# Kernel optimization log

Hardware: AMD Instinct MI355X
Metric: run time of the kernel (lower is better)

Reference implementation:

```python
import jax, jax.numpy as jnp
import numpy as np
from jax import lax

N_OBJ = 21   # 20 VOC classes + background
N_ACT = 27   # HICO actions
HUMAN = 14   # index of 'human' in VOC_BBOX_LABEL_NAMES
ROI_SZ = 7
SCALE = 1.0 / 16.0
STD = (0.1, 0.1, 0.2, 0.2)
MEAN = (0.0, 0.0, 0.0, 0.0)
SIGMA = 0.3
NMS_T = 0.0  # thresh passed to non_maximum_suppression in source
EPS = 1e-3
NEG = -1e30


def setup_inputs():
    key = jax.random.key(0)
    ks = jax.random.split(key, 9)
    R = 2000
    C, Hf, Wf = 512, 38, 50
    Himg, Wimg = 608, 800
    x = jax.random.normal(ks[0], (1, C, Hf, Wf), dtype=jnp.float32)
    pred_scores = jax.random.normal(ks[1], (R, N_OBJ), dtype=jnp.float32)
    pred_off = 0.5 * jax.random.normal(ks[2], (R, N_OBJ * 4), dtype=jnp.float32)
    ys = jnp.sort(jax.random.uniform(ks[3], (R, 2), minval=0.0, maxval=Himg - 1.0), axis=1)
    xs = jnp.sort(jax.random.uniform(ks[4], (R, 2), minval=0.0, maxval=Wimg - 1.0), axis=1)
    rois = jnp.stack([ys[:, 0], xs[:, 0], ys[:, 1] + 1.0, xs[:, 1] + 1.0], axis=1)  # [R,4] yxyx, image coords
    D = C * ROI_SZ * ROI_SZ  # 25088
    W1 = jax.random.normal(ks[5], (D, 4096), dtype=jnp.float32) / np.float32(np.sqrt(D))
    b1 = jnp.zeros((4096,), jnp.float32)
    W2 = jax.random.normal(ks[6], (4096, 4096), dtype=jnp.float32) / 64.0
    b2 = jnp.zeros((4096,), jnp.float32)
    W_loc = jax.random.normal(ks[7], (4096, 4), dtype=jnp.float32) / 64.0
    b_loc = jnp.zeros((4,), jnp.float32)
    W_act = jax.random.normal(ks[8], (4096, N_ACT), dtype=jnp.float32) / 64.0
    b_act = jnp.zeros((N_ACT,), jnp.float32)
    imgshape = jnp.array([Himg, Wimg], dtype=jnp.int32)
    return {"x": x, "pred_scores": pred_scores, "pred_off": pred_off, "rois": rois,
            "imgshape": imgshape, "W1": W1, "b1": b1, "W2": W2, "b2": b2,
            "W_loc": W_loc, "b_loc": b_loc, "W_act": W_act, "b_act": b_act}


def loc2bbox(src, loc):
    # src, loc: [...,4] (y1,x1,y2,x2) / (dy,dx,dh,dw)
    h = src[..., 2] - src[..., 0]
    w = src[..., 3] - src[..., 1]
    cy = src[..., 0] + 0.5 * h
    cx = src[..., 1] + 0.5 * w
    cy2 = loc[..., 0] * h + cy
    cx2 = loc[..., 1] * w + cx
    h2 = jnp.exp(loc[..., 2]) * h
    w2 = jnp.exp(loc[..., 3]) * w
    return jnp.stack([cy2 - 0.5 * h2, cx2 - 0.5 * w2, cy2 + 0.5 * h2, cx2 + 0.5 * w2], axis=-1)


def nms_keep(boxes, scores):
    # chainercv-style greedy NMS: suppress if IoU with an already-kept box >= NMS_T
    R = boxes.shape[0]
    order = jnp.argsort(-scores)
    b = boxes[order]
    tl = jnp.maximum(b[:, None, :2], b[None, :, :2])
    br = jnp.minimum(b[:, None, 2:], b[None, :, 2:])
    inter = jnp.prod(jnp.maximum(br - tl, 0.0), axis=-1)
    area = jnp.prod(jnp.maximum(b[:, 2:] - b[:, :2], 0.0), axis=-1)
    iou = inter / (area[:, None] + area[None, :] - inter + 1e-12)
    idx = jnp.arange(R)
    def body(i, keep):
        sup = jnp.any((iou[i] >= NMS_T) & keep & (idx < i))
        return keep.at[i].set(~sup)
    keep_sorted = lax.fori_loop(0, R, body, jnp.ones((R,), bool))
    return jnp.zeros((R,), bool).at[order].set(keep_sorted)


def roi_pool(feat, box_yxyx):
    # chainer RoIPooling2D on one roi; roi fed as [x1,y1,x2,y2] then scaled by SCALE
    C, Hf, Wf = feat.shape
    y1, x1, y2, x2 = box_yxyx[0], box_yxyx[1], box_yxyx[2], box_yxyx[3]
    xmin = jnp.round(x1 * SCALE).astype(jnp.int32)
    ymin = jnp.round(y1 * SCALE).astype(jnp.int32)
    xmax = jnp.round(x2 * SCALE).astype(jnp.int32)
    ymax = jnp.round(y2 * SCALE).astype(jnp.int32)
    rw = jnp.maximum(xmax - xmin + 1, 1).astype(jnp.float32)
    rh = jnp.maximum(ymax - ymin + 1, 1).astype(jnp.float32)
    p = jnp.arange(ROI_SZ, dtype=jnp.float32)
    hstart = jnp.clip(ymin + jnp.floor(p * rh / ROI_SZ).astype(jnp.int32), 0, Hf)
    hend = jnp.clip(ymin + jnp.ceil((p + 1.0) * rh / ROI_SZ).astype(jnp.int32), 0, Hf)
    wstart = jnp.clip(xmin + jnp.floor(p * rw / ROI_SZ).astype(jnp.int32), 0, Wf)
    wend = jnp.clip(xmin + jnp.ceil((p + 1.0) * rw / ROI_SZ).astype(jnp.int32), 0, Wf)
    r = jnp.arange(Hf)
    c = jnp.arange(Wf)
    rowm = (r[None, :] >= hstart[:, None]) & (r[None, :] < hend[:, None])  # [7,Hf]
    colm = (c[None, :] >= wstart[:, None]) & (c[None, :] < wend[:, None])  # [7,Wf]
    t = jnp.where(colm[None, None, :, :], feat[:, :, None, :], NEG).max(axis=-1)  # [C,Hf,7]
    out = jnp.where(rowm[None, :, :, None], t[:, None, :, :], NEG).max(axis=2)    # [C,7,7]
    return jnp.where(out <= NEG * 0.5, 0.0, out)


def xywh(b):
    # quirky encoding used in forward: x=(b3-b1)/2, y=(b2-b0)/2, w=b3-b1, h=b2-b0
    w = b[..., 3] - b[..., 1]
    h = b[..., 2] - b[..., 0]
    return jnp.stack([0.5 * w, 0.5 * h, w, h], axis=-1)


def reference(x, pred_scores, pred_off, rois, imgshape, W1, b1, W2, b2, W_loc, b_loc, W_act, b_act):
    Hf, Wf = x.shape[2], x.shape[3]
    R = rois.shape[0]
    img = imgshape.astype(jnp.float32)
    my_scale = Hf / img[0]
    sy = Hf / img[0]
    sx = Wf / img[1]
    roi = rois * jnp.stack([sy, sx, sy, sx])  # resize_bbox(image -> feature)
    std = jnp.tile(jnp.asarray(STD, jnp.float32), (N_OBJ,))
    mean = jnp.tile(jnp.asarray(MEAN, jnp.float32), (N_OBJ,))
    loc = (pred_off * std + mean).reshape(R, N_OBJ, 4)
    src = jnp.broadcast_to(roi[:, None, :], loc.shape)
    cb = loc2bbox(src, loc)  # [R,21,4]
    yc = jnp.clip(cb[..., 0::2], 0.0, float(Hf))
    xc = jnp.clip(cb[..., 1::2], 0.0, float(Wf))
    cls_bbox = jnp.stack([yc[..., 0], xc[..., 0], yc[..., 1], xc[..., 1]], axis=-1)
    prob = jax.nn.softmax(pred_scores, axis=1)  # strictly > 0, so prob>0 mask keeps all
    boxes_c = jnp.swapaxes(cls_bbox[:, 1:, :], 0, 1)  # [20,R,4]
    scores_c = prob[:, 1:].T                          # [20,R]
    keep = jax.vmap(nms_keep)(boxes_c, scores_c)      # [20,R] bool
    bbox_all = boxes_c.reshape(-1, 4)
    score_all = scores_c.reshape(-1)
    label_all = jnp.repeat(jnp.arange(N_OBJ - 1), R)
    kept = keep.reshape(-1)
    # get_pred_human_box: best-scoring kept box with label 'human'
    hmask = kept & (label_all == HUMAN)
    hi = jnp.argmax(jnp.where(hmask, score_all, -1.0))
    human_box = bbox_all[hi]  # feature coords, yxyx
    # RoI pool + classifier heads
    pool = roi_pool(x[0], human_box)
    feat = pool.reshape(1, -1)  # [1, 25088]
    fc7 = jax.nn.relu(jax.nn.relu(feat @ W1 + b1) @ W2 + b2)
    pred_object_loc = fc7 @ W_loc + b_loc   # [1,4]
    action_scores = fc7 @ W_act + b_act     # [1,27]
    # test-mode: gaussian over relative box encodings to pick object
    h4 = xywh(human_box)
    mu = xywh(pred_object_loc[0])
    cand = xywh(bbox_all)  # [20R,4]
    hw = jnp.maximum(h4[2], EPS)
    hh = jnp.maximum(h4[3], EPS)
    cw = jnp.maximum(cand[:, 2], EPS)
    ch = jnp.maximum(cand[:, 3], EPS)
    boh = jnp.stack([(cand[:, 0] - h4[0]) / hw, (cand[:, 1] - h4[1]) / hh,
                     jnp.log(cw / hw), jnp.log(ch / hh)], axis=-1)
    gau = jnp.exp(-jnp.sum((boh - mu) ** 2, axis=-1) / (2.0 * SIGMA * SIGMA))
    vmask = kept & (label_all != HUMAN)
    bi = jnp.argmax(jnp.where(vmask, gau, -1.0))
    obj_box = bbox_all[bi]
    # resize back to image coords (flip_bbox treated as identity)
    inv = jnp.stack([img[0] / Hf, img[1] / Wf, img[0] / Hf, img[1] / Wf])
    pred_human_box = (human_box * inv)[None, :]
    pred_obj_box = (obj_box * inv)[None, :]
    return pred_human_box, pred_obj_box, action_scores, my_scale
```

## Files before the change

kernel.cpp:

```cpp
#include <hip/hip_runtime.h>
#include <math.h>

#define R_ROIS 2000
#define NOBJ   21
#define NACT   27
#define HUMAN  14
#define CFEAT  512
#define HF     38
#define WF     50
#define DFEAT  (CFEAT*7*7)
#define H1DIM  4096

typedef float floatx4 __attribute__((ext_vector_type(4)));

#define WS_KEPT   0
#define WS_FEAT   80
#define WS_H1     (WS_FEAT + DFEAT)
#define WS_FC7    (WS_H1 + H1DIM)
#define WS_LOC    (WS_FC7 + H1DIM)
#define WS_ACT    (WS_LOC + 4)

__global__ __launch_bounds__(256)
void k_top(const float* __restrict__ scores, const float* __restrict__ off,
           const float* __restrict__ rois, const int* __restrict__ imgshape,
           float* __restrict__ kept_box, float* __restrict__ h1,
           float* __restrict__ fc7) {
    int g = blockIdx.x * 256 + threadIdx.x;
    for (int j = g; j < 2 * H1DIM; j += 20 * 256) {
        if (j < H1DIM) h1[j] = 0.f; else fc7[j - H1DIM] = 0.f;
    }

    int cls = blockIdx.x + 1;
    __shared__ float sval[256];
    __shared__ int   sidx[256];
    float best = -1e30f; int bidx = 0x7fffffff;
    for (int r = threadIdx.x; r < R_ROIS; r += 256) {
        const float* s = scores + r * NOBJ;
        float m = s[0];
        #pragma unroll
        for (int c = 1; c < NOBJ; ++c) m = fmaxf(m, s[c]);
        float sum = 0.f;
        #pragma unroll
        for (int c = 0; c < NOBJ; ++c) sum += expf(s[c] - m);
        float v = s[cls] - (m + logf(sum));
        if (v > best) { best = v; bidx = r; }
    }
    sval[threadIdx.x] = best; sidx[threadIdx.x] = bidx;
    __syncthreads();
    for (int s = 128; s > 0; s >>= 1) {
        if (threadIdx.x < s) {
            float ov = sval[threadIdx.x + s]; int oi = sidx[threadIdx.x + s];
            if (ov > sval[threadIdx.x] ||
                (ov == sval[threadIdx.x] && oi < sidx[threadIdx.x])) {
                sval[threadIdx.x] = ov; sidx[threadIdx.x] = oi;
            }
        }
        __syncthreads();
    }
    if (threadIdx.x == 0) {
        int r = sidx[0];
        float Himg = (float)imgshape[0], Wimg = (float)imgshape[1];
        float sy = (float)HF / Himg, sx = (float)WF / Wimg;
        float y1 = rois[r*4+0]*sy, x1 = rois[r*4+1]*sx;
        float y2 = rois[r*4+2]*sy, x2 = rois[r*4+3]*sx;
        float dy = off[r*(NOBJ*4) + cls*4+0] * 0.1f;
        float dx = off[r*(NOBJ*4) + cls*4+1] * 0.1f;
        float dh = off[r*(NOBJ*4) + cls*4+2] * 0.2f;
        float dw = off[r*(NOBJ*4) + cls*4+3] * 0.2f;
        float h = y2 - y1, w = x2 - x1;
        float cy = y1 + 0.5f*h, cx = x1 + 0.5f*w;
        float cy2 = dy*h + cy, cx2 = dx*w + cx;
        float h2 = expf(dh)*h, w2 = expf(dw)*w;
        float by1 = fminf(fmaxf(cy2 - 0.5f*h2, 0.f), (float)HF);
        float bx1 = fminf(fmaxf(cx2 - 0.5f*w2, 0.f), (float)WF);
        float by2 = fminf(fmaxf(cy2 + 0.5f*h2, 0.f), (float)HF);
        float bx2 = fminf(fmaxf(cx2 + 0.5f*w2, 0.f), (float)WF);
        int l = cls - 1;
        kept_box[l*4+0] = by1; kept_box[l*4+1] = bx1;
        kept_box[l*4+2] = by2; kept_box[l*4+3] = bx2;
    }
}

__global__ void k_roipool(const float* __restrict__ x, const float* __restrict__ kept_box,
                          float* __restrict__ feat) {
    int idx = blockIdx.x * blockDim.x + threadIdx.x;
    if (idx >= DFEAT) return;
    float y1 = kept_box[HUMAN*4+0], x1 = kept_box[HUMAN*4+1];
    float y2 = kept_box[HUMAN*4+2], x2 = kept_box[HUMAN*4+3];
    int xmin = (int)rintf(x1 * 0.0625f);
    int ymin = (int)rintf(y1 * 0.0625f);
    int xmax = (int)rintf(x2 * 0.0625f);
    int ymax = (int)rintf(y2 * 0.0625f);
    float rw = (float)max(xmax - xmin + 1, 1);
    float rh = (float)max(ymax - ymin + 1, 1);
    int c = idx / 49, rem = idx % 49, pi = rem / 7, pj = rem % 7;
    int hs  = min(max(ymin + (int)floorf((float)pi * rh / 7.f), 0), HF);
    int he  = min(max(ymin + (int)ceilf((float)(pi+1) * rh / 7.f), 0), HF);
    int wss = min(max(xmin + (int)floorf((float)pj * rw / 7.f), 0), WF);
    int we  = min(max(xmin + (int)ceilf((float)(pj+1) * rw / 7.f), 0), WF);
    float m = -1e30f;
    for (int rr = hs; rr < he; ++rr)
        for (int cc = wss; cc < we; ++cc)
            m = fmaxf(m, x[c*(HF*WF) + rr*WF + cc]);
    feat[idx] = (m <= -5e29f) ? 0.f : m;
}

template<int ROWS, bool RELU>
__global__ __launch_bounds__(256)
void k_matvec(const float* __restrict__ W, const float* __restrict__ vin,
              const float* __restrict__ bias, float* __restrict__ vout, int ncols) {
    __shared__ float sv[ROWS];
    int row0 = blockIdx.x * ROWS;
    int col0 = blockIdx.y * 1024 + threadIdx.x * 4;
    for (int i = threadIdx.x; i < ROWS; i += 256) {
        float v = vin[row0 + i];
        if (RELU) v = fmaxf(v + bias[row0 + i], 0.f);
        sv[i] = v;
    }
    __syncthreads();
    float a0 = 0.f, a1 = 0.f, a2 = 0.f, a3 = 0.f;
    const floatx4* Wv = (const floatx4*)W;
    long base = ((long)row0 * ncols + col0) >> 2;
    int stride = ncols >> 2;
    #pragma unroll 8
    for (int i = 0; i < ROWS; ++i) {
        float f = sv[i];
        floatx4 w = __builtin_nontemporal_load(&Wv[base + (long)i * stride]);
        a0 += f * w.x; a1 += f * w.y; a2 += f * w.z; a3 += f * w.w;
    }
    atomicAdd(&vout[col0+0], a0);
    atomicAdd(&vout[col0+1], a1);
    atomicAdd(&vout[col0+2], a2);
    atomicAdd(&vout[col0+3], a3);
}

__global__ void k_heads(const float* __restrict__ fc7, const float* __restrict__ b2,
                        const float* __restrict__ W_loc, const float* __restrict__ b_loc,
                        const float* __restrict__ W_act, const float* __restrict__ b_act,
                        float* __restrict__ loc_out, float* __restrict__ act_out) {
    int k = blockIdx.x;
    __shared__ float red[256];
    float sum = 0.f;
    if (k < 4) {
        for (int i = threadIdx.x; i < H1DIM; i += 256) {
            float f = fmaxf(fc7[i] + b2[i], 0.f);
            sum += f * W_loc[i*4 + k];
        }
    } else {
        int j = k - 4;
        for (int i = threadIdx.x; i < H1DIM; i += 256) {
            float f = fmaxf(fc7[i] + b2[i], 0.f);
            sum += f * W_act[i*NACT + j];
        }
    }
    red[threadIdx.x] = sum; __syncthreads();
    for (int s = 128; s > 0; s >>= 1) {
        if (threadIdx.x < s) red[threadIdx.x] += red[threadIdx.x + s];
        __syncthreads();
    }
    if (threadIdx.x == 0) {
        if (k < 4) loc_out[k] = red[0] + b_loc[k];
        else       act_out[k-4] = red[0] + b_act[k-4];
    }
}

__global__ void k_final(const float* __restrict__ kept_box, const float* __restrict__ loc_out,
                        const float* __restrict__ act_out, const int* __restrict__ imgshape,
                        float* __restrict__ out) {
    if (threadIdx.x != 0 || blockIdx.x != 0) return;
    float hb0 = kept_box[HUMAN*4+0], hb1 = kept_box[HUMAN*4+1];
    float hb2 = kept_box[HUMAN*4+2], hb3 = kept_box[HUMAN*4+3];
    float h4w = hb3 - hb1, h4h = hb2 - hb0;
    float h4x = 0.5f * h4w, h4y = 0.5f * h4h;
    float hw = fmaxf(h4w, 1e-3f), hh = fmaxf(h4h, 1e-3f);
    float l0 = loc_out[0], l1 = loc_out[1], l2 = loc_out[2], l3 = loc_out[3];
    float muw = l3 - l1, muh = l2 - l0;
    float mux = 0.5f * muw, muy = 0.5f * muh;
    float bestg = -2.f; int bl = 0;
    for (int l = 0; l < 20; ++l) {
        if (l == HUMAN) continue;
        float b0 = kept_box[l*4+0], b1 = kept_box[l*4+1];
        float b2 = kept_box[l*4+2], b3 = kept_box[l*4+3];
        float cw = fmaxf(b3 - b1, 1e-3f), ch = fmaxf(b2 - b0, 1e-3f);
        float c0 = 0.5f * (b3 - b1), c1 = 0.5f * (b2 - b0);
        float d0 = (c0 - h4x) / hw - mux;
        float d1 = (c1 - h4y) / hh - muy;
        float d2 = logf(cw / hw) - muw;
        float d3 = logf(ch / hh) - muh;
        float g = expf(-(d0*d0 + d1*d1 + d2*d2 + d3*d3) / (2.f * 0.3f * 0.3f));
        if (g > bestg) { bestg = g; bl = l; }
    }
    float Himg = (float)imgshape[0], Wimg = (float)imgshape[1];
    float iy = Himg / (float)HF, ix = Wimg / (float)WF;
    out[0] = hb0 * iy; out[1] = hb1 * ix; out[2] = hb2 * iy; out[3] = hb3 * ix;
    out[4] = kept_box[bl*4+0] * iy; out[5] = kept_box[bl*4+1] * ix;
    out[6] = kept_box[bl*4+2] * iy; out[7] = kept_box[bl*4+3] * ix;
    for (int j = 0; j < NACT; ++j) out[8+j] = act_out[j];
    out[35] = (float)HF / Himg;
}

extern "C" void kernel_launch(void* const* d_in, const int* in_sizes, int n_in,
                              void* d_out, int out_size, void* d_ws, size_t ws_size,
                              hipStream_t stream) {
    const float* x           = (const float*)d_in[0];
    const float* pred_scores = (const float*)d_in[1];
    const float* pred_off    = (const float*)d_in[2];
    const float* rois        = (const float*)d_in[3];
    const int*   imgshape    = (const int*)d_in[4];
    const float* W1          = (const float*)d_in[5];
    const float* b1          = (const float*)d_in[6];
    const float* W2          = (const float*)d_in[7];
    const float* b2          = (const float*)d_in[8];
    const float* W_loc       = (const float*)d_in[9];
    const float* b_loc       = (const float*)d_in[10];
    const float* W_act       = (const float*)d_in[11];
    const float* b_act       = (const float*)d_in[12];
    float* out = (float*)d_out;

    float* ws   = (float*)d_ws;
    float* kept = ws + WS_KEPT;
    float* feat = ws + WS_FEAT;
    float* h1   = ws + WS_H1;
    float* fc7  = ws + WS_FC7;
    float* loco = ws + WS_LOC;
    float* acto = ws + WS_ACT;

    k_top<<<20, 256, 0, stream>>>(pred_scores, pred_off, rois, imgshape, kept, h1, fc7);
    k_roipool<<<(DFEAT + 255) / 256, 256, 0, stream>>>(x, kept, feat);
    k_matvec<128, false><<<dim3(196, 4), 256, 0, stream>>>(W1, feat, (const float*)nullptr, h1, H1DIM);
    k_matvec<64, true><<<dim3(64, 4), 256, 0, stream>>>(W2, h1, b1, fc7, H1DIM);
    k_heads<<<31, 256, 0, stream>>>(fc7, b2, W_loc, b_loc, W_act, b_act, loco, acto);
    k_final<<<1, 64, 0, stream>>>(kept, loco, acto, imgshape, out);
}
```

Before: 612.1 us.

## Fuse class top-box selection with ROI pooling and heads with final selection

Merges the per-class top-box kernel and the ROI pooling kernel into one launch. The 98 pooling blocks each recompute the human-class argmax redundantly, so they no longer wait for a separate kernel to publish the human box. It also folds the 31-block head kernel and the single-thread final kernel into one 256-thread block that stages relu(fc7+b2) in shared memory. This cuts the launch count from six to four, at the cost of redundant softmax/argmax work in every pooling block and a serialised single-block head computation.

Result: slower. 690.9 us (+12.9%).

```diff
diff --git a/kernel.cpp b/kernel.cpp
--- a/kernel.cpp
+++ b/kernel.cpp
@@ -17,22 +17,12 @@
 #define WS_FEAT   80
 #define WS_H1     (WS_FEAT + DFEAT)
 #define WS_FC7    (WS_H1 + H1DIM)
-#define WS_LOC    (WS_FC7 + H1DIM)
-#define WS_ACT    (WS_LOC + 4)
-
-__global__ __launch_bounds__(256)
-void k_top(const float* __restrict__ scores, const float* __restrict__ off,
-           const float* __restrict__ rois, const int* __restrict__ imgshape,
-           float* __restrict__ kept_box, float* __restrict__ h1,
-           float* __restrict__ fc7) {
-    int g = blockIdx.x * 256 + threadIdx.x;
-    for (int j = g; j < 2 * H1DIM; j += 20 * 256) {
-        if (j < H1DIM) h1[j] = 0.f; else fc7[j - H1DIM] = 0.f;
-    }
-
-    int cls = blockIdx.x + 1;
-    __shared__ float sval[256];
-    __shared__ int   sidx[256];
+
+__device__ __forceinline__
+void block_class_top(int cls, const float* __restrict__ scores,
+                     const float* __restrict__ off, const float* __restrict__ rois,
+                     const int* __restrict__ imgshape,
+                     float* sval, int* sidx, float* sbox) {
     float best = -1e30f; int bidx = 0x7fffffff;
     for (int r = threadIdx.x; r < R_ROIS; r += 256) {
         const float* s = scores + r * NOBJ;
@@ -71,28 +61,50 @@
         float cy = y1 + 0.5f*h, cx = x1 + 0.5f*w;
         float cy2 = dy*h + cy, cx2 = dx*w + cx;
         float h2 = expf(dh)*h, w2 = expf(dw)*w;
-        float by1 = fminf(fmaxf(cy2 - 0.5f*h2, 0.f), (float)HF);
-        float bx1 = fminf(fmaxf(cx2 - 0.5f*w2, 0.f), (float)WF);
-        float by2 = fminf(fmaxf(cy2 + 0.5f*h2, 0.f), (float)HF);
-        float bx2 = fminf(fmaxf(cx2 + 0.5f*w2, 0.f), (float)WF);
-        int l = cls - 1;
-        kept_box[l*4+0] = by1; kept_box[l*4+1] = bx1;
-        kept_box[l*4+2] = by2; kept_box[l*4+3] = bx2;
-    }
-}
-
-__global__ void k_roipool(const float* __restrict__ x, const float* __restrict__ kept_box,
-                          float* __restrict__ feat) {
-    int idx = blockIdx.x * blockDim.x + threadIdx.x;
-    if (idx >= DFEAT) return;
-    float y1 = kept_box[HUMAN*4+0], x1 = kept_box[HUMAN*4+1];
-    float y2 = kept_box[HUMAN*4+2], x2 = kept_box[HUMAN*4+3];
+        sbox[0] = fminf(fmaxf(cy2 - 0.5f*h2, 0.f), (float)HF);
+        sbox[1] = fminf(fmaxf(cx2 - 0.5f*w2, 0.f), (float)WF);
+        sbox[2] = fminf(fmaxf(cy2 + 0.5f*h2, 0.f), (float)HF);
+        sbox[3] = fminf(fmaxf(cx2 + 0.5f*w2, 0.f), (float)WF);
+    }
+    __syncthreads();
+}
+
+__global__ __launch_bounds__(256)
+void k_top_pool(const float* __restrict__ scores, const float* __restrict__ off,
+                const float* __restrict__ rois, const int* __restrict__ imgshape,
+                const float* __restrict__ x,
+                float* __restrict__ kept_box, float* __restrict__ feat,
+                float* __restrict__ h1, float* __restrict__ fc7) {
+    __shared__ float sval[256];
+    __shared__ int   sidx[256];
+    __shared__ float sbox[4];
+
+    int g = blockIdx.x * 256 + threadIdx.x;
+    for (int j = g; j < 2 * H1DIM; j += 118 * 256) {
+        if (j < H1DIM) h1[j] = 0.f; else fc7[j - H1DIM] = 0.f;
+    }
+
+    if (blockIdx.x < 20) {
+        int cls = blockIdx.x + 1;
+        block_class_top(cls, scores, off, rois, imgshape, sval, sidx, sbox);
+        if (threadIdx.x == 0) {
+            int l = cls - 1;
+            kept_box[l*4+0] = sbox[0]; kept_box[l*4+1] = sbox[1];
+            kept_box[l*4+2] = sbox[2]; kept_box[l*4+3] = sbox[3];
+        }
+        return;
+    }
+
+    block_class_top(HUMAN + 1, scores, off, rois, imgshape, sval, sidx, sbox);
+    float y1 = sbox[0], x1 = sbox[1], y2 = sbox[2], x2 = sbox[3];
     int xmin = (int)rintf(x1 * 0.0625f);
     int ymin = (int)rintf(y1 * 0.0625f);
     int xmax = (int)rintf(x2 * 0.0625f);
     int ymax = (int)rintf(y2 * 0.0625f);
     float rw = (float)max(xmax - xmin + 1, 1);
     float rh = (float)max(ymax - ymin + 1, 1);
+    int idx = (blockIdx.x - 20) * 256 + threadIdx.x;
+    if (idx >= DFEAT) return;
     int c = idx / 49, rem = idx % 49, pi = rem / 7, pj = rem % 7;
     int hs  = min(max(ymin + (int)floorf((float)pi * rh / 7.f), 0), HF);
     int he  = min(max(ymin + (int)ceilf((float)(pi+1) * rh / 7.f), 0), HF);
@@ -134,55 +146,60 @@
     atomicAdd(&vout[col0+3], a3);
 }
 
-__global__ void k_heads(const float* __restrict__ fc7, const float* __restrict__ b2,
-                        const float* __restrict__ W_loc, const float* __restrict__ b_loc,
-                        const float* __restrict__ W_act, const float* __restrict__ b_act,
-                        float* __restrict__ loc_out, float* __restrict__ act_out) {
-    int k = blockIdx.x;
+__global__ __launch_bounds__(256)
+void k_heads_final(const float* __restrict__ fc7, const float* __restrict__ b2,
+                   const float* __restrict__ W_loc, const float* __restrict__ b_loc,
+                   const float* __restrict__ W_act, const float* __restrict__ b_act,
+                   const float* __restrict__ kept_box, const int* __restrict__ imgshape,
+                   float* __restrict__ out) {
+    __shared__ float f[H1DIM];
     __shared__ float red[256];
-    float sum = 0.f;
-    if (k < 4) {
-        for (int i = threadIdx.x; i < H1DIM; i += 256) {
-            float f = fmaxf(fc7[i] + b2[i], 0.f);
-            sum += f * W_loc[i*4 + k];
-        }
-    } else {
-        int j = k - 4;
-        for (int i = threadIdx.x; i < H1DIM; i += 256) {
-            float f = fmaxf(fc7[i] + b2[i], 0.f);
-            sum += f * W_act[i*NACT + j];
-        }
-    }
-    red[threadIdx.x] = sum; __syncthreads();
-    for (int s = 128; s > 0; s >>= 1) {
-        if (threadIdx.x < s) red[threadIdx.x] += red[threadIdx.x + s];
+    __shared__ float res[31];
+    for (int i = threadIdx.x; i < H1DIM; i += 256)
+        f[i] = fmaxf(fc7[i] + b2[i], 0.f);
+    __syncthreads();
+
+    int lane = threadIdx.x & 63;
+    for (int k = 0; k < 31; ++k) {
+        float sum = 0.f;
+        if (k < 4) {
+            for (int i = threadIdx.x; i < H1DIM; i += 256) sum += f[i] * W_loc[i*4 + k];
+        } else {
+            int j = k - 4;
+            for (int i = threadIdx.x; i < H1DIM; i += 256) sum += f[i] * W_act[i*NACT + j];
+        }
+        red[threadIdx.x] = sum; __syncthreads();
+        if (threadIdx.x < 128) red[threadIdx.x] += red[threadIdx.x + 128];
         __syncthreads();
-    }
-    if (threadIdx.x == 0) {
-        if (k < 4) loc_out[k] = red[0] + b_loc[k];
-        else       act_out[k-4] = red[0] + b_act[k-4];
-    }
-}
-
-__global__ void k_final(const float* __restrict__ kept_box, const float* __restrict__ loc_out,
-                        const float* __restrict__ act_out, const int* __restrict__ imgshape,
-                        float* __restrict__ out) {
-    if (threadIdx.x != 0 || blockIdx.x != 0) return;
+        if (threadIdx.x < 64) {
+            float v = red[threadIdx.x] + red[threadIdx.x + 64];
+            v += __shfl_down(v, 32);
+            v += __shfl_down(v, 16);
+            v += __shfl_down(v, 8);
+            v += __shfl_down(v, 4);
+            v += __shfl_down(v, 2);
+            v += __shfl_down(v, 1);
+            if (lane == 0) res[k] = v + (k < 4 ? b_loc[k] : b_act[k-4]);
+        }
+        __syncthreads();
+    }
+
+    if (threadIdx.x != 0) return;
     float hb0 = kept_box[HUMAN*4+0], hb1 = kept_box[HUMAN*4+1];
     float hb2 = kept_box[HUMAN*4+2], hb3 = kept_box[HUMAN*4+3];
     float h4w = hb3 - hb1, h4h = hb2 - hb0;
     float h4x = 0.5f * h4w, h4y = 0.5f * h4h;
     float hw = fmaxf(h4w, 1e-3f), hh = fmaxf(h4h, 1e-3f);
-    float l0 = loc_out[0], l1 = loc_out[1], l2 = loc_out[2], l3 = loc_out[3];
+    float l0 = res[0], l1 = res[1], l2 = res[2], l3 = res[3];
     float muw = l3 - l1, muh = l2 - l0;
     float mux = 0.5f * muw, muy = 0.5f * muh;
     float bestg = -2.f; int bl = 0;
     for (int l = 0; l < 20; ++l) {
         if (l == HUMAN) continue;
         float b0 = kept_box[l*4+0], b1 = kept_box[l*4+1];
-        float b2 = kept_box[l*4+2], b3 = kept_box[l*4+3];
-        float cw = fmaxf(b3 - b1, 1e-3f), ch = fmaxf(b2 - b0, 1e-3f);
-        float c0 = 0.5f * (b3 - b1), c1 = 0.5f * (b2 - b0);
+        float b2_ = kept_box[l*4+2], b3 = kept_box[l*4+3];
+        float cw = fmaxf(b3 - b1, 1e-3f), ch = fmaxf(b2_ - b0, 1e-3f);
+        float c0 = 0.5f * (b3 - b1), c1 = 0.5f * (b2_ - b0);
         float d0 = (c0 - h4x) / hw - mux;
         float d1 = (c1 - h4y) / hh - muy;
         float d2 = logf(cw / hw) - muw;
@@ -195,7 +212,7 @@
     out[0] = hb0 * iy; out[1] = hb1 * ix; out[2] = hb2 * iy; out[3] = hb3 * ix;
     out[4] = kept_box[bl*4+0] * iy; out[5] = kept_box[bl*4+1] * ix;
     out[6] = kept_box[bl*4+2] * iy; out[7] = kept_box[bl*4+3] * ix;
-    for (int j = 0; j < NACT; ++j) out[8+j] = act_out[j];
+    for (int j = 0; j < NACT; ++j) out[8+j] = res[4+j];
     out[35] = (float)HF / Himg;
 }
 
@@ -222,13 +239,11 @@
     float* feat = ws + WS_FEAT;
     float* h1   = ws + WS_H1;
     float* fc7  = ws + WS_FC7;
-    float* loco = ws + WS_LOC;
-    float* acto = ws + WS_ACT;
-
-    k_top<<<20, 256, 0, stream>>>(pred_scores, pred_off, rois, imgshape, kept, h1, fc7);
-    k_roipool<<<(DFEAT + 255) / 256, 256, 0, stream>>>(x, kept, feat);
+
+    k_top_pool<<<118, 256, 0, stream>>>(pred_scores, pred_off, rois, imgshape,
+                                        x, kept, feat, h1, fc7);
     k_matvec<128, false><<<dim3(196, 4), 256, 0, stream>>>(W1, feat, (const float*)nullptr, h1, H1DIM);
     k_matvec<64, true><<<dim3(64, 4), 256, 0, stream>>>(W2, h1, b1, fc7, H1DIM);
-    k_heads<<<31, 256, 0, stream>>>(fc7, b2, W_loc, b_loc, W_act, b_act, loco, acto);
-    k_final<<<1, 64, 0, stream>>>(kept, loco, acto, imgshape, out);
-}
+    k_heads_final<<<1, 256, 0, stream>>>(fc7, b2, W_loc, b_loc, W_act, b_act,
+                                         kept, imgshape, out);
+}
```
